# Optimization experiments

Hardware: AMD Instinct MI355X
Metric: run time of the kernel (lower is better)

The kernel has to match this reference:

```python
import jax, jax.numpy as jnp
from jax import lax
import numpy as np

HEADS = 8
DIM_HEAD = 64


def setup_inputs() -> dict:
    key = jax.random.key(0)
    ks = jax.random.split(key, 6)
    dim, inner = 256, HEADS * DIM_HEAD
    fmap = jax.random.normal(ks[0], (8, dim, 128, 128), dtype=jnp.float32)
    w_q = jax.random.normal(ks[1], (inner, dim), dtype=jnp.float32) * (dim ** -0.5)
    w_dw = jax.random.normal(ks[2], (dim, 1, 3, 3), dtype=jnp.float32) * (9 ** -0.5)
    w_pw = jax.random.normal(ks[3], (2 * inner, dim), dtype=jnp.float32) * (dim ** -0.5)
    w_out = jax.random.normal(ks[4], (dim, inner), dtype=jnp.float32) * (inner ** -0.5)
    b_out = jnp.zeros((dim,), dtype=jnp.float32)
    return {"fmap": fmap, "w_q": w_q, "w_dw": w_dw, "w_pw": w_pw, "w_out": w_out, "b_out": b_out}


def _linear_attention(fmap, w_q, w_dw, w_pw, w_out, b_out):
    B, C, H, W = fmap.shape
    h, d = HEADS, DIM_HEAD
    scale = d ** -0.5
    N = H * W
    # to_q: 1x1 conv, no bias
    q = jnp.einsum('bcxy,oc->boxy', fmap, w_q)  # [B, h*d, H, W]
    # to_kv: depthwise 3x3 (pad 1) then pointwise 1x1, no bias
    dw = lax.conv_general_dilated(
        fmap, w_dw, window_strides=(1, 1), padding=((1, 1), (1, 1)),
        dimension_numbers=('NCHW', 'OIHW', 'NCHW'), feature_group_count=C)
    kv = jnp.einsum('bcxy,oc->boxy', dw, w_pw)  # [B, 2*h*d, H, W]
    k, v = jnp.split(kv, 2, axis=1)

    def to_bhnc(t):  # b (h c) x y -> (b h) (x y) c
        return t.reshape(B, h, d, N).transpose(0, 1, 3, 2).reshape(B * h, N, d)

    q, k, v = to_bhnc(q), to_bhnc(k), to_bhnc(v)
    q = jax.nn.softmax(q, axis=-1) * scale  # softmax over feature dim
    k = jax.nn.softmax(k, axis=-2)          # softmax over spatial dim
    context = jnp.einsum('bnd,bne->bde', k, v)   # [(B*h), d, d]
    out = jnp.einsum('bnd,bde->bne', q, context)  # [(B*h), N, d]
    # (b h) (x y) d -> b (h d) x y
    out = out.reshape(B, h, N, d).transpose(0, 1, 3, 2).reshape(B, h * d, H, W)
    out = jax.nn.gelu(out, approximate=False)
    out = jnp.einsum('bcxy,oc->boxy', out, w_out) + b_out[None, :, None, None]
    return out


def reference(fmap, w_q, w_dw, w_pw, w_out, b_out):
    return _linear_attention(fmap, w_q, w_dw, w_pw, w_out, b_out)
```

## Files before the change

kernel.cpp:

```cpp
#include <hip/hip_runtime.h>
#include <math.h>

#define NPIX 16384

typedef __bf16 bf16x8 __attribute__((ext_vector_type(8)));
typedef float f32x4 __attribute__((ext_vector_type(4)));
typedef unsigned short u16;
typedef unsigned int u32;

__device__ __forceinline__ u16 f2bf(float f) {
    u32 u = __float_as_uint(f);
    u32 r = (u + 0x7FFFu + ((u >> 16) & 1u)) >> 16;
    return (u16)r;
}
__device__ __forceinline__ float bf2f(u32 s) { return __uint_as_float(s << 16); }
__device__ __forceinline__ u32 pk2(float a, float b) {
    return (u32)f2bf(a) | ((u32)f2bf(b) << 16);
}

__global__ __launch_bounds__(256) void k_cvtw(
    const float* __restrict__ wq, const float* __restrict__ wpw,
    const float* __restrict__ wout,
    u16* __restrict__ wq_b, u16* __restrict__ wpw_b, u16* __restrict__ wout_b)
{
    int id = (blockIdx.x * 256 + threadIdx.x) * 4;
    const float* s; u16* d; int off;
    if (id < 131072)      { s = wq;   d = wq_b;   off = id; }
    else if (id < 393216) { s = wpw;  d = wpw_b;  off = id - 131072; }
    else                  { s = wout; d = wout_b; off = id - 393216; }
    f32x4 v = *(const f32x4*)(s + off);
    uint2 u; u.x = pk2(v[0], v[1]); u.y = pk2(v[2], v[3]);
    *(uint2*)(d + off) = u;
}

__global__ __launch_bounds__(256) void k_conv(
    const float* __restrict__ fmap, const float* __restrict__ wdw,
    u16* __restrict__ fmapT, u16* __restrict__ dwT)
{
    const int t = threadIdx.x;
    const int lane = t & 63, w = t >> 6;
    const int x = blockIdx.x, b = blockIdx.y;

    __shared__ u16 dst[2][128][66];

    const float mLf = (lane == 0) ? 0.f : 1.f;
    const float mRf = (lane == 63) ? 0.f : 1.f;
    const float mTf = (x > 0) ? 1.f : 0.f;
    const float mBf = (x < 127) ? 1.f : 0.f;
    const int dT = (x > 0) ? -128 : 0;
    const int dB = (x < 127) ? 128 : 0;

    const size_t nbase = (size_t)b * NPIX + (size_t)x * 128;

    for (int chunk = 0; chunk < 4; ++chunk) {
        for (int g = 0; g < 4; ++g) {
            const int cl0 = w * 16 + g * 4;
            const int c0 = chunk * 64 + cl0;
            float2 T[4], M[4], B[4];
            #pragma unroll
            for (int i = 0; i < 4; ++i) {
                const float* p = fmap + ((size_t)(b * 256 + c0 + i)) * NPIX + (size_t)x * 128;
                M[i] = ((const float2*)p)[lane];
                T[i] = ((const float2*)(p + dT))[lane];
                B[i] = ((const float2*)(p + dB))[lane];
            }
            #pragma unroll
            for (int i = 0; i < 4; ++i) {
                const float* wc = wdw + (c0 + i) * 9;
                float w0 = wc[0] * mTf, w1 = wc[1] * mTf, w2 = wc[2] * mTf;
                float w3 = wc[3],       w4 = wc[4],       w5 = wc[5];
                float w6 = wc[6] * mBf, w7 = wc[7] * mBf, w8 = wc[8] * mBf;
                float tL = __shfl_up(T[i].y, 1) * mLf;
                float mL_ = __shfl_up(M[i].y, 1) * mLf;
                float bL = __shfl_up(B[i].y, 1) * mLf;
                float tR = __shfl_down(T[i].x, 1) * mRf;
                float mR_ = __shfl_down(M[i].x, 1) * mRf;
                float bR = __shfl_down(B[i].x, 1) * mRf;
                float o0 = w0 * tL     + w1 * T[i].x + w2 * T[i].y
                         + w3 * mL_    + w4 * M[i].x + w5 * M[i].y
                         + w6 * bL     + w7 * B[i].x + w8 * B[i].y;
                float o1 = w0 * T[i].x + w1 * T[i].y + w2 * tR
                         + w3 * M[i].x + w4 * M[i].y + w5 * mR_
                         + w6 * B[i].x + w7 * B[i].y + w8 * bR;
                int cl = cl0 + i;
                dst[0][2 * lane][cl]     = f2bf(M[i].x);
                dst[0][2 * lane + 1][cl] = f2bf(M[i].y);
                dst[1][2 * lane][cl]     = f2bf(o0);
                dst[1][2 * lane + 1][cl] = f2bf(o1);
            }
        }
        __syncthreads();
        #pragma unroll
        for (int T2 = 0; T2 < 2; ++T2) {
            u16* gp = T2 ? dwT : fmapT;
            #pragma unroll
            for (int it = 0; it < 4; ++it) {
                int u = it * 256 + t;
                int y = u >> 3, c8 = (u & 7) * 8;
                const u16* s = &dst[T2][y][c8];
                uint4 val;
                val.x = *(const u32*)(s);
                val.y = *(const u32*)(s + 2);
                val.z = *(const u32*)(s + 4);
                val.w = *(const u32*)(s + 6);
                *(uint4*)(gp + (nbase + y) * 256 + chunk * 64 + c8) = val;
            }
        }
        __syncthreads();
    }
}

__global__ __launch_bounds__(256, 3) void k_kvctx(
    const u16* __restrict__ dwT, const u16* __restrict__ wpw,
    float* __restrict__ ctx, float* __restrict__ denom)
{
    const int t = threadIdx.x;
    const int lane = t & 63, w = t >> 6;
    const int l15 = lane & 15, quad = lane >> 4;

    const int L = blockIdx.x;
    const int work = (L & 7) * 128 + (L >> 3);
    const int s = work >> 6;
    const int b = (work >> 3) & 7;
    const int h = work & 7;
    const int bh = b * 8 + h;

    __shared__ __align__(16) u16 As[128 * 72];
    __shared__ __align__(16) u16 Bs[128 * 72];
    u16* EL = As;
    u16* VL = Bs;

    const int ph = (w & 1) * 64;
    const int ck = (w >> 1);

    f32x4 ctxacc[4] = {};
    float dpart[4] = {0.f, 0.f, 0.f, 0.f};

    for (int st = 0; st < 8; ++st) {
        const int n0 = s * 1024 + st * 128;
        const u16* xrow = dwT + ((size_t)b * NPIX + n0) * 256;
        f32x4 acc[4][4] = {};
        for (int kc = 0; kc < 4; ++kc) {
            __syncthreads();
            const int g = t & 7;
            #pragma unroll
            for (int p = 0; p < 4; ++p) {
                int row = (t >> 3) + 32 * p;
                int wr = (row < 64) ? (h * 64 + row) : (512 + h * 64 + (row - 64));
                *(uint4*)(As + row * 72 + g * 8) = *(const uint4*)(wpw + (size_t)wr * 256 + kc * 64 + g * 8);
                *(uint4*)(Bs + row * 72 + g * 8) = *(const uint4*)(xrow + (size_t)row * 256 + kc * 64 + g * 8);
            }
            __syncthreads();
            #pragma unroll
            for (int kk = 0; kk < 64; kk += 32) {
                bf16x8 av[4], bv[4];
                #pragma unroll
                for (int mf = 0; mf < 4; ++mf)
                    av[mf] = *(const bf16x8*)(Bs + (ph + mf * 16 + l15) * 72 + kk + quad * 8);
                #pragma unroll
                for (int nf = 0; nf < 4; ++nf)
                    bv[nf] = *(const bf16x8*)(As + (ck * 64 + nf * 16 + l15) * 72 + kk + quad * 8);
                #pragma unroll
                for (int mf = 0; mf < 4; ++mf)
                    #pragma unroll
                    for (int nf = 0; nf < 4; ++nf)
                        acc[mf][nf] = __builtin_amdgcn_mfma_f32_16x16x32_bf16(av[mf], bv[nf], acc[mf][nf], 0, 0, 0);
            }
        }
        __syncthreads();
        u16* dst = ck ? VL : EL;
        #pragma unroll
        for (int nf = 0; nf < 4; ++nf) {
            const int ch = nf * 16 + l15;
            float colsum = 0.f;
            #pragma unroll
            for (int mf = 0; mf < 4; ++mf) {
                const int px = ph + mf * 16 + quad * 4;
                float v0 = acc[mf][nf][0], v1 = acc[mf][nf][1];
                float v2 = acc[mf][nf][2], v3 = acc[mf][nf][3];
                if (ck == 0) {
                    v0 = __expf(v0); v1 = __expf(v1);
                    v2 = __expf(v2); v3 = __expf(v3);
                    colsum += (v0 + v1) + (v2 + v3);
                }
                uint2 u; u.x = pk2(v0, v1); u.y = pk2(v2, v3);
                *(uint2*)(dst + ch * 136 + px) = u;
            }
            if (ck == 0) {
                colsum += __shfl_xor(colsum, 16);
                colsum += __shfl_xor(colsum, 32);
                dpart[nf] += colsum;
            }
        }
        __syncthreads();
        #pragma unroll
        for (int kk2 = 0; kk2 < 128; kk2 += 32) {
            bf16x8 av = *(const bf16x8*)(VL + (w * 16 + l15) * 136 + kk2 + quad * 8);
            #pragma unroll
            for (int nf = 0; nf < 4; ++nf) {
                bf16x8 bv = *(const bf16x8*)(EL + (nf * 16 + l15) * 136 + kk2 + quad * 8);
                ctxacc[nf] = __builtin_amdgcn_mfma_f32_16x16x32_bf16(av, bv, ctxacc[nf], 0, 0, 0);
            }
        }
    }
    #pragma unroll
    for (int nf = 0; nf < 4; ++nf)
        #pragma unroll
        for (int r = 0; r < 4; ++r) {
            int e = w * 16 + quad * 4 + r;
            int d = nf * 16 + l15;
            atomicAdd(ctx + ((size_t)bh * 64 + e) * 64 + d, ctxacc[nf][r]);
        }
    if (ck == 0 && quad == 0) {
        #pragma unroll
        for (int nf = 0; nf < 4; ++nf)
            atomicAdd(denom + bh * 64 + nf * 16 + l15, dpart[nf]);
    }
}

__global__ __launch_bounds__(256) void k_proj_q(
    const u16* __restrict__ fmapT, const u16* __restrict__ wq,
    u16* __restrict__ q)
{
    const int t = threadIdx.x;
    const int lane = t & 63, w = t >> 6;
    const int l15 = lane & 15, quad = lane >> 4;
    const int n0 = blockIdx.x * 128;
    const int o0 = blockIdx.y * 128;
    const int b  = blockIdx.z;
    __shared__ __align__(16) unsigned char smraw[71680];
    u16* As = (u16*)smraw;
    u16* Bs = As + 128 * 72;
    f32x4 acc[4][4] = {};
    const int mh = (w >> 1) * 64, nh = (w & 1) * 64;
    const u16* wrow = wq + (size_t)o0 * 256;
    const u16* xrow = fmapT + ((size_t)b * NPIX + n0) * 256;
    for (int kc = 0; kc < 4; ++kc) {
        __syncthreads();
        const int g = t & 7;
        #pragma unroll
        for (int p = 0; p < 4; ++p) {
            int row = (t >> 3) + 32 * p;
            *(uint4*)(As + row * 72 + g * 8) = *(const uint4*)(wrow + (size_t)row * 256 + kc * 64 + g * 8);
            *(uint4*)(Bs + row * 72 + g * 8) = *(const uint4*)(xrow + (size_t)row * 256 + kc * 64 + g * 8);
        }
        __syncthreads();
        #pragma unroll
        for (int kk = 0; kk < 64; kk += 32) {
            bf16x8 av[4], bv[4];
            #pragma unroll
            for (int mf = 0; mf < 4; ++mf)
                av[mf] = *(const bf16x8*)(As + (mh + mf * 16 + l15) * 72 + kk + quad * 8);
            #pragma unroll
            for (int nf = 0; nf < 4; ++nf)
                bv[nf] = *(const bf16x8*)(Bs + (nh + nf * 16 + l15) * 72 + kk + quad * 8);
            #pragma unroll
            for (int mf = 0; mf < 4; ++mf)
                #pragma unroll
                for (int nf = 0; nf < 4; ++nf)
                    acc[mf][nf] = __builtin_amdgcn_mfma_f32_16x16x32_bf16(av[mf], bv[nf], acc[mf][nf], 0, 0, 0);
        }
    }
    __syncthreads();
    float* ep = (float*)smraw;
    #pragma unroll
    for (int mf = 0; mf < 4; ++mf)
        #pragma unroll
        for (int nf = 0; nf < 4; ++nf)
            #pragma unroll
            for (int r = 0; r < 4; ++r) {
                int row = mh + mf * 16 + quad * 4 + r;
                int col = nh + nf * 16 + l15;
                ep[col * 140 + row] = acc[mf][nf][r];
            }
    __syncthreads();
    const int h0 = blockIdx.y * 2;
    for (int p = 0; p < 8; ++p) {
        int unit = p * 32 + (t >> 3);
        int pix = unit >> 1, hh = unit & 1;
        int d8 = (t & 7) * 8;
        f32x4 v0 = *(const f32x4*)(ep + pix * 140 + hh * 64 + d8);
        f32x4 v1 = *(const f32x4*)(ep + pix * 140 + hh * 64 + d8 + 4);
        float e0 = __expf(v0[0]), e1 = __expf(v0[1]), e2 = __expf(v0[2]), e3 = __expf(v0[3]);
        float e4 = __expf(v1[0]), e5 = __expf(v1[1]), e6 = __expf(v1[2]), e7 = __expf(v1[3]);
        float s = ((e0 + e1) + (e2 + e3)) + ((e4 + e5) + (e6 + e7));
        s += __shfl_xor(s, 1); s += __shfl_xor(s, 2); s += __shfl_xor(s, 4);
        float r = 0.125f / s;
        uint4 u;
        u.x = pk2(e0 * r, e1 * r); u.y = pk2(e2 * r, e3 * r);
        u.z = pk2(e4 * r, e5 * r); u.w = pk2(e6 * r, e7 * r);
        size_t off = (((size_t)b * 8 + h0 + hh) * NPIX + n0 + pix) * 64 + d8;
        *(uint4*)(q + off) = u;
    }
}

__global__ __launch_bounds__(256) void k_attnout(
    const u16* __restrict__ q, const float* __restrict__ ctx,
    const float* __restrict__ denom, const u16* __restrict__ wout,
    const float* __restrict__ bout, float* __restrict__ out)
{
    const int t = threadIdx.x;
    const int lane = t & 63, w = t >> 6;
    const int l15 = lane & 15, quad = lane >> 4;
    const int n0 = blockIdx.x * 32;
    const int b  = blockIdx.y;
    __shared__ __align__(16) u16 tmp[32 * 520];
    __shared__ __align__(16) unsigned char R[20480];
    u16* qs = (u16*)R;
    u16* cs = (u16*)(R + 4608);
    u16* ws = (u16*)R;
    for (int h = 0; h < 8; ++h) {
        __syncthreads();
        {
            int row = t >> 3, g = t & 7;
            *(uint4*)(qs + row * 72 + g * 8) =
                *(const uint4*)(q + (((size_t)b * 8 + h) * NPIX + n0 + row) * 64 + g * 8);
        }
        const int bh = b * 8 + h;
        #pragma unroll
        for (int p = 0; p < 4; ++p) {
            int idx = p * 256 + t;
            int e = idx >> 4, dq = (idx & 15) * 4;
            f32x4 c4 = *(const f32x4*)(ctx + ((size_t)bh * 64 + e) * 64 + dq);
            f32x4 d4 = *(const f32x4*)(denom + bh * 64 + dq);
            uint2 u;
            u.x = pk2(c4[0] / d4[0], c4[1] / d4[1]);
            u.y = pk2(c4[2] / d4[2], c4[3] / d4[3]);
            *(uint2*)(cs + e * 72 + dq) = u;
        }
        __syncthreads();
        f32x4 a1[2] = {};
        #pragma unroll
        for (int kk = 0; kk < 64; kk += 32) {
            bf16x8 av = *(const bf16x8*)(qs + ((w & 1) * 16 + l15) * 72 + kk + quad * 8);
            #pragma unroll
            for (int j = 0; j < 2; ++j) {
                int nf = (w >> 1) * 2 + j;
                bf16x8 bv = *(const bf16x8*)(cs + (nf * 16 + l15) * 72 + kk + quad * 8);
                a1[j] = __builtin_amdgcn_mfma_f32_16x16x32_bf16(av, bv, a1[j], 0, 0, 0);
            }
        }
        #pragma unroll
        for (int j = 0; j < 2; ++j)
            #pragma unroll
            for (int r = 0; r < 4; ++r) {
                int pix = (w & 1) * 16 + quad * 4 + r;
                int e = ((w >> 1) * 2 + j) * 16 + l15;
                float x = a1[j][r];
                float gel = 0.5f * x * (1.0f + erff(x * 0.70710678118654752f));
                tmp[pix * 520 + h * 64 + e] = f2bf(gel);
            }
    }
    __syncthreads();
    f32x4 acc[4][2] = {};
    for (int kc = 0; kc < 16; ++kc) {
        __syncthreads();
        #pragma unroll
        for (int p = 0; p < 4; ++p) {
            int c = (t >> 2) + 64 * p, g = t & 3;
            *(uint4*)(ws + c * 40 + g * 8) = *(const uint4*)(wout + (size_t)c * 512 + kc * 32 + g * 8);
        }
        __syncthreads();
        bf16x8 av[4], bv[2];
        #pragma unroll
        for (int mf = 0; mf < 4; ++mf)
            av[mf] = *(const bf16x8*)(ws + (w * 64 + mf * 16 + l15) * 40 + quad * 8);
        #pragma unroll
        for (int nf = 0; nf < 2; ++nf)
            bv[nf] = *(const bf16x8*)(tmp + (nf * 16 + l15) * 520 + kc * 32 + quad * 8);
        #pragma unroll
        for (int mf = 0; mf < 4; ++mf)
            #pragma unroll
            for (int nf = 0; nf < 2; ++nf)
                acc[mf][nf] = __builtin_amdgcn_mfma_f32_16x16x32_bf16(av[mf], bv[nf], acc[mf][nf], 0, 0, 0);
    }
    #pragma unroll
    for (int mf = 0; mf < 4; ++mf)
        #pragma unroll
        for (int nf = 0; nf < 2; ++nf)
            #pragma unroll
            for (int r = 0; r < 4; ++r) {
                int c = w * 64 + mf * 16 + quad * 4 + r;
                int pix = nf * 16 + l15;
                out[((size_t)b * 256 + c) * NPIX + n0 + pix] = acc[mf][nf][r] + bout[c];
            }
}

extern "C" void kernel_launch(void* const* d_in, const int* in_sizes, int n_in,
                              void* d_out, int out_size, void* d_ws, size_t ws_size,
                              hipStream_t stream)
{
    const float* fmap  = (const float*)d_in[0];
    const float* w_q   = (const float*)d_in[1];
    const float* w_dw  = (const float*)d_in[2];
    const float* w_pw  = (const float*)d_in[3];
    const float* w_out = (const float*)d_in[4];
    const float* b_out = (const float*)d_in[5];
    float* out = (float*)d_out;
    char* ws = (char*)d_ws;

    u16* dwT     = (u16*)(ws);
    u16* fmapT   = (u16*)(ws + 67108864);
    u16* q       = (u16*)(ws + 134217728);
    float* ctx   = (float*)(ws + 402653184);
    float* denom = (float*)(ws + 403701760);
    u16* wq_b    = (u16*)(ws + 403718144);
    u16* wpw_b   = (u16*)(ws + 403980288);
    u16* wout_b  = (u16*)(ws + 404504576);

    hipMemsetAsync(ws + 402653184, 0, 1048576 + 16384, stream);
    k_cvtw<<<512, 256, 0, stream>>>(w_q, w_pw, w_out, wq_b, wpw_b, wout_b);
    k_conv<<<dim3(128, 8), 256, 0, stream>>>(fmap, w_dw, fmapT, dwT);
    k_kvctx<<<1024, 256, 0, stream>>>(dwT, wpw_b, ctx, denom);
    k_proj_q<<<dim3(128, 4, 8), 256, 0, stream>>>(fmapT, wq_b, q);
    k_attnout<<<dim3(512, 8), 256, 0, stream>>>(q, ctx, denom, wout_b, b_out, out);
}
```

Before: 782.3 us.

## Double-buffer and XOR-swizzle LDS tiles in kvctx and proj_q GEMMs

Both GEMM kernels now use register-staged double buffering: the next k-chunk's global loads are issued before the MFMAs on the current chunk, and the data is written to the alternate LDS buffer afterward. The padded 72-stride layout is replaced by an XOR-swizzled 64-stride layout to avoid bank conflicts, and the kvctx E/V tiles get the same swizzle. This aims to hide global load latency and remove a barrier per chunk. The cost is higher LDS use (64KB in kvctx), with occupancy lowered from 3 to 2 blocks, and more register pressure.

After: 735.3 us. 1.06x faster.

```diff
diff --git a/kernel.cpp b/kernel.cpp
--- a/kernel.cpp
+++ b/kernel.cpp
@@ -110,7 +110,7 @@
     }
 }
 
-__global__ __launch_bounds__(256, 3) void k_kvctx(
+__global__ __launch_bounds__(256, 2) void k_kvctx(
     const u16* __restrict__ dwT, const u16* __restrict__ wpw,
     float* __restrict__ ctx, float* __restrict__ denom)
 {
@@ -125,46 +125,83 @@
     const int h = work & 7;
     const int bh = b * 8 + h;
 
-    __shared__ __align__(16) u16 As[128 * 72];
-    __shared__ __align__(16) u16 Bs[128 * 72];
-    u16* EL = As;
-    u16* VL = Bs;
+    __shared__ __align__(16) u16 sm[32768];
+    u16* EL = sm;
+    u16* VL = sm + 8192;
 
     const int ph = (w & 1) * 64;
     const int ck = (w >> 1);
 
+    const int srow = t >> 3;
+    const int sg = t & 7;
+
     f32x4 ctxacc[4] = {};
     float dpart[4] = {0.f, 0.f, 0.f, 0.f};
 
+    uint4 ra[4], rb[4];
+
+#define KV_STAGE_LOAD(stv, kcv)                                                        \
+    {                                                                                  \
+        const u16* xr = dwT + ((size_t)b * NPIX + s * 1024 + (stv) * 128) * 256;       \
+        _Pragma("unroll")                                                              \
+        for (int p = 0; p < 4; ++p) {                                                  \
+            int row = srow + 32 * p;                                                   \
+            int wr = (row < 64) ? (h * 64 + row) : (512 + h * 64 + (row - 64));        \
+            ra[p] = *(const uint4*)(wpw + (size_t)wr * 256 + (kcv) * 64 + sg * 8);     \
+            rb[p] = *(const uint4*)(xr + (size_t)row * 256 + (kcv) * 64 + sg * 8);     \
+        }                                                                              \
+    }
+
+#define KV_STAGE_WRITE(bufi)                                                           \
+    {                                                                                  \
+        u16* Ad = sm + (bufi) * 8192;                                                  \
+        u16* Bd = sm + 16384 + (bufi) * 8192;                                          \
+        _Pragma("unroll")                                                              \
+        for (int p = 0; p < 4; ++p) {                                                  \
+            int row = srow + 32 * p;                                                   \
+            int off = row * 64 + ((sg ^ (row & 7)) << 3);                              \
+            *(uint4*)(Ad + off) = ra[p];                                               \
+            *(uint4*)(Bd + off) = rb[p];                                               \
+        }                                                                              \
+    }
+
+    KV_STAGE_LOAD(0, 0);
+
     for (int st = 0; st < 8; ++st) {
-        const int n0 = s * 1024 + st * 128;
-        const u16* xrow = dwT + ((size_t)b * NPIX + n0) * 256;
+        KV_STAGE_WRITE(0);
+        __syncthreads();
         f32x4 acc[4][4] = {};
+        #pragma unroll
         for (int kc = 0; kc < 4; ++kc) {
-            __syncthreads();
-            const int g = t & 7;
-            #pragma unroll
-            for (int p = 0; p < 4; ++p) {
-                int row = (t >> 3) + 32 * p;
-                int wr = (row < 64) ? (h * 64 + row) : (512 + h * 64 + (row - 64));
-                *(uint4*)(As + row * 72 + g * 8) = *(const uint4*)(wpw + (size_t)wr * 256 + kc * 64 + g * 8);
-                *(uint4*)(Bs + row * 72 + g * 8) = *(const uint4*)(xrow + (size_t)row * 256 + kc * 64 + g * 8);
-            }
-            __syncthreads();
-            #pragma unroll
-            for (int kk = 0; kk < 64; kk += 32) {
-                bf16x8 av[4], bv[4];
+            if (kc < 3) KV_STAGE_LOAD(st, kc + 1);
+            {
+                const u16* Ax = sm + (kc & 1) * 8192;
+                const u16* Bx = sm + 16384 + (kc & 1) * 8192;
                 #pragma unroll
-                for (int mf = 0; mf < 4; ++mf)
-                    av[mf] = *(const bf16x8*)(Bs + (ph + mf * 16 + l15) * 72 + kk + quad * 8);
-                #pragma unroll
-                for (int nf = 0; nf < 4; ++nf)
-                    bv[nf] = *(const bf16x8*)(As + (ck * 64 + nf * 16 + l15) * 72 + kk + quad * 8);
-                #pragma unroll
-                for (int mf = 0; mf < 4; ++mf)
+                for (int kk = 0; kk < 64; kk += 32) {
+                    bf16x8 av[4], bv[4];
                     #pragma unroll
-                    for (int nf = 0; nf < 4; ++nf)
-                        acc[mf][nf] = __builtin_amdgcn_mfma_f32_16x16x32_bf16(av[mf], bv[nf], acc[mf][nf], 0, 0, 0);
+                    for (int mf = 0; mf < 4; ++mf) {
+                        int pr = ph + mf * 16 + l15;
+                        int pg = ((kk >> 3) + quad) ^ (pr & 7);
+                        av[mf] = *(const bf16x8*)(Bx + pr * 64 + (pg << 3));
+                    }
+                    #pragma unroll
+                    for (int nf = 0; nf < 4; ++nf) {
+                        int wr2 = ck * 64 + nf * 16 + l15;
+                        int wg = ((kk >> 3) + quad) ^ (wr2 & 7);
+                        bv[nf] = *(const bf16x8*)(Ax + wr2 * 64 + (wg << 3));
+                    }
+                    #pragma unroll
+                    for (int mf = 0; mf < 4; ++mf)
+                        #pragma unroll
+                        for (int nf = 0; nf < 4; ++nf)
+                            acc[mf][nf] = __builtin_amdgcn_mfma_f32_16x16x32_bf16(av[mf], bv[nf], acc[mf][nf], 0, 0, 0);
+                }
+            }
+            if (kc < 3) {
+                KV_STAGE_WRITE((kc + 1) & 1);
+                __syncthreads();
             }
         }
         __syncthreads();
@@ -172,10 +209,11 @@
         #pragma unroll
         for (int nf = 0; nf < 4; ++nf) {
             const int ch = nf * 16 + l15;
+            const int key = ch & 7;
             float colsum = 0.f;
             #pragma unroll
             for (int mf = 0; mf < 4; ++mf) {
-                const int px = ph + mf * 16 + quad * 4;
+                const int c = ph + mf * 16 + quad * 4;
                 float v0 = acc[mf][nf][0], v1 = acc[mf][nf][1];
                 float v2 = acc[mf][nf][2], v3 = acc[mf][nf][3];
                 if (ck == 0) {
@@ -184,7 +222,8 @@
                     colsum += (v0 + v1) + (v2 + v3);
                 }
                 uint2 u; u.x = pk2(v0, v1); u.y = pk2(v2, v3);
-                *(uint2*)(dst + ch * 136 + px) = u;
+                int addr = ch * 128 + ((((c >> 3) ^ key)) << 3) + (c & 7);
+                *(uint2*)(dst + addr) = u;
             }
             if (ck == 0) {
                 colsum += __shfl_xor(colsum, 16);
@@ -192,16 +231,22 @@
                 dpart[nf] += colsum;
             }
         }
+        if (st < 7) KV_STAGE_LOAD(st + 1, 0);
         __syncthreads();
         #pragma unroll
         for (int kk2 = 0; kk2 < 128; kk2 += 32) {
-            bf16x8 av = *(const bf16x8*)(VL + (w * 16 + l15) * 136 + kk2 + quad * 8);
+            int ar = w * 16 + l15;
+            int ag = ((kk2 >> 3) + quad) ^ (ar & 7);
+            bf16x8 av = *(const bf16x8*)(VL + ar * 128 + (ag << 3));
             #pragma unroll
             for (int nf = 0; nf < 4; ++nf) {
-                bf16x8 bv = *(const bf16x8*)(EL + (nf * 16 + l15) * 136 + kk2 + quad * 8);
+                int br = nf * 16 + l15;
+                int bg = ((kk2 >> 3) + quad) ^ (br & 7);
+                bf16x8 bv = *(const bf16x8*)(EL + br * 128 + (bg << 3));
                 ctxacc[nf] = __builtin_amdgcn_mfma_f32_16x16x32_bf16(av, bv, ctxacc[nf], 0, 0, 0);
             }
         }
+        __syncthreads();
     }
     #pragma unroll
     for (int nf = 0; nf < 4; ++nf)
@@ -216,6 +261,8 @@
         for (int nf = 0; nf < 4; ++nf)
             atomicAdd(denom + bh * 64 + nf * 16 + l15, dpart[nf]);
     }
+#undef KV_STAGE_LOAD
+#undef KV_STAGE_WRITE
 }
 
 __global__ __launch_bounds__(256) void k_proj_q(
@@ -229,36 +276,72 @@
     const int o0 = blockIdx.y * 128;
     const int b  = blockIdx.z;
     __shared__ __align__(16) unsigned char smraw[71680];
-    u16* As = (u16*)smraw;
-    u16* Bs = As + 128 * 72;
+    u16* sm16 = (u16*)smraw;
     f32x4 acc[4][4] = {};
     const int mh = (w >> 1) * 64, nh = (w & 1) * 64;
     const u16* wrow = wq + (size_t)o0 * 256;
     const u16* xrow = fmapT + ((size_t)b * NPIX + n0) * 256;
+    const int srow = t >> 3;
+    const int sg = t & 7;
+    uint4 ra[4], rb[4];
+
+#define Q_STAGE_LOAD(kcv)                                                              \
+    {                                                                                  \
+        _Pragma("unroll")                                                              \
+        for (int p = 0; p < 4; ++p) {                                                  \
+            int row = srow + 32 * p;                                                   \
+            ra[p] = *(const uint4*)(wrow + (size_t)row * 256 + (kcv) * 64 + sg * 8);   \
+            rb[p] = *(const uint4*)(xrow + (size_t)row * 256 + (kcv) * 64 + sg * 8);   \
+        }                                                                              \
+    }
+
+#define Q_STAGE_WRITE(bufi)                                                            \
+    {                                                                                  \
+        u16* Ad = sm16 + (bufi) * 8192;                                                \
+        u16* Bd = sm16 + 16384 + (bufi) * 8192;                                        \
+        _Pragma("unroll")                                                              \
+        for (int p = 0; p < 4; ++p) {                                                  \
+            int row = srow + 32 * p;                                                   \
+            int off = row * 64 + ((sg ^ (row & 7)) << 3);                              \
+            *(uint4*)(Ad + off) = ra[p];                                               \
+            *(uint4*)(Bd + off) = rb[p];                                               \
+        }                                                                              \
+    }
+
+    Q_STAGE_LOAD(0);
+    Q_STAGE_WRITE(0);
+    __syncthreads();
+    #pragma unroll
     for (int kc = 0; kc < 4; ++kc) {
-        __syncthreads();
-        const int g = t & 7;
-        #pragma unroll
-        for (int p = 0; p < 4; ++p) {
-            int row = (t >> 3) + 32 * p;
-            *(uint4*)(As + row * 72 + g * 8) = *(const uint4*)(wrow + (size_t)row * 256 + kc * 64 + g * 8);
-            *(uint4*)(Bs + row * 72 + g * 8) = *(const uint4*)(xrow + (size_t)row * 256 + kc * 64 + g * 8);
-        }
-        __syncthreads();
-        #pragma unroll
-        for (int kk = 0; kk < 64; kk += 32) {
-            bf16x8 av[4], bv[4];
-            #pragma unroll
-            for (int mf = 0; mf < 4; ++mf)
-                av[mf] = *(const bf16x8*)(As + (mh + mf * 16 + l15) * 72 + kk + quad * 8);
-            #pragma unroll
-            for (int nf = 0; nf < 4; ++nf)
-                bv[nf] = *(const bf16x8*)(Bs + (nh + nf * 16 + l15) * 72 + kk + quad * 8);
-            #pragma unroll
-            for (int mf = 0; mf < 4; ++mf)
+        if (kc < 3) Q_STAGE_LOAD(kc + 1);
+        {
+            const u16* Ax = sm16 + (kc & 1) * 8192;
+            const u16* Bx = sm16 + 16384 + (kc & 1) * 8192;
+            #pragma unroll
+            for (int kk = 0; kk < 64; kk += 32) {
+                bf16x8 av[4], bv[4];
                 #pragma unroll
-                for (int nf = 0; nf < 4; ++nf)
-                    acc[mf][nf] = __builtin_amdgcn_mfma_f32_16x16x32_bf16(av[mf], bv[nf], acc[mf][nf], 0, 0, 0);
+                for (int mf = 0; mf < 4; ++mf) {
+                    int arow = mh + mf * 16 + l15;
+                    int agr = ((kk >> 3) + quad) ^ (arow & 7);
+                    av[mf] = *(const bf16x8*)(Ax + arow * 64 + (agr << 3));
+                }
+                #pragma unroll
+                for (int nf = 0; nf < 4; ++nf) {
+                    int brow = nh + nf * 16 + l15;
+                    int bgr = ((kk >> 3) + quad) ^ (brow & 7);
+                    bv[nf] = *(const bf16x8*)(Bx + brow * 64 + (bgr << 3));
+                }
+                #pragma unroll
+                for (int mf = 0; mf < 4; ++mf)
+                    #pragma unroll
+                    for (int nf = 0; nf < 4; ++nf)
+                        acc[mf][nf] = __builtin_amdgcn_mfma_f32_16x16x32_bf16(av[mf], bv[nf], acc[mf][nf], 0, 0, 0);
+            }
+        }
+        if (kc < 3) {
+            Q_STAGE_WRITE((kc + 1) & 1);
+            __syncthreads();
         }
     }
     __syncthreads();
@@ -292,6 +375,8 @@
         size_t off = (((size_t)b * 8 + h0 + hh) * NPIX + n0 + pix) * 64 + d8;
         *(uint4*)(q + off) = u;
     }
+#undef Q_STAGE_LOAD
+#undef Q_STAGE_WRITE
 }
 
 __global__ __launch_bounds__(256) void k_attnout(
```
